# Kernel optimization log

Hardware: AMD Instinct MI355X
Metric: run time of the kernel (lower is better)

The kernel has to match this reference:

```python
import jax, jax.numpy as jnp
import numpy as np

HEADS = 16
D_MODEL = 1024
MAX_LEN = 1024
BATCH = 4
SEQ = 1024


def _skew(QEr):
    # Transformer-XL / Music-Transformer skew trick.
    # QEr: [B, H, L, L] -> pad one zero column on the left, reshape, drop first row.
    B, H, L, _ = QEr.shape
    padded = jnp.pad(QEr, ((0, 0), (0, 0), (0, 0), (1, 0)))  # [B,H,L,L+1]
    reshaped = padded.reshape(B, H, L + 1, L)
    return reshaped[:, :, 1:, :]  # [B,H,L,L]


def setup_inputs() -> dict:
    key = jax.random.key(0)
    ks = jax.random.split(key, 8)
    d = D_MODEL // HEADS
    std = 0.05  # tf.random_normal_initializer default stddev
    return {
        "query": jax.random.normal(ks[0], (BATCH, SEQ, D_MODEL), jnp.float32),
        "key": jax.random.normal(ks[1], (BATCH, SEQ, D_MODEL), jnp.float32),
        "value": jax.random.normal(ks[2], (BATCH, SEQ, D_MODEL), jnp.float32),
        "WQ": std * jax.random.normal(ks[3], (D_MODEL, D_MODEL), jnp.float32),
        "WK": std * jax.random.normal(ks[4], (D_MODEL, D_MODEL), jnp.float32),
        "WV": std * jax.random.normal(ks[5], (D_MODEL, D_MODEL), jnp.float32),
        "Er": std * jax.random.normal(ks[6], (MAX_LEN, d), jnp.float32),
        "WMerge": std * jax.random.normal(ks[7], (D_MODEL, D_MODEL), jnp.float32),
    }


def reference(query, key, value, WQ, WK, WV, Er, WMerge):
    B, L, D = query.shape
    H = HEADS
    d = D // H
    # Faithful to source: plain reshape (NOT transpose-based head split).
    q = (query @ WQ).reshape(B, H, L, d)          # [B,H,L,d]
    k_t = (key @ WK).reshape(B, H, d, L)          # [B,H,d,L]
    v = (value @ WV).reshape(B, H, L, d)          # [B,H,L,d]
    start = MAX_LEN - L
    Er_t = Er[start:, :].T                        # [d, L]
    QEr = q @ Er_t                                # [B,H,L,L]
    Srel = _skew(QEr)                             # [B,H,L,L]
    attn = (q @ k_t + Srel) / jnp.sqrt(jnp.asarray(d, q.dtype))
    attn = jax.nn.softmax(attn, axis=-1)
    out = attn @ v                                # [B,H,L,d]
    out = out.transpose(0, 2, 1, 3).reshape(B, L, D)
    return out @ WMerge
```

## Files before the change

### kernel.cpp

```cpp
#include <hip/hip_runtime.h>

#define H_  16
#define L_  1024
#define D_  1024
#define DH  64

typedef short bf16x8 __attribute__((ext_vector_type(8)));
typedef float f32x4  __attribute__((ext_vector_type(4)));

__device__ __forceinline__ ushort f2bf(float f) {
  union { float f; unsigned int u; } x; x.f = f;
  unsigned int u = x.u;
  u = (u + 0x7fffu + ((u >> 16) & 1u)) >> 16;
  return (ushort)u;
}
__device__ __forceinline__ float bf2f(ushort s) {
  union { unsigned int u; float f; } x; x.u = ((unsigned int)s) << 16;
  return x.f;
}

__global__ __launch_bounds__(256) void erF_kernel(const float* __restrict__ Er,
                                                  ushort* __restrict__ ErF) {
  int t = blockIdx.x * 256 + threadIdx.x;
  int lane = t & 63, ph = (t >> 6) & 1, jg = t >> 7;
  int m = jg * 16 + (lane & 15);
  int k = ph * 32 + (lane >> 4) * 8;
  float4 f0 = *(const float4*)(Er + m * 64 + k);
  float4 f1 = *(const float4*)(Er + m * 64 + k + 4);
  ushort4 u0, u1;
  u0.x = f2bf(f0.x); u0.y = f2bf(f0.y); u0.z = f2bf(f0.z); u0.w = f2bf(f0.w);
  u1.x = f2bf(f1.x); u1.y = f2bf(f1.y); u1.z = f2bf(f1.z); u1.w = f2bf(f1.w);
  *(ushort4*)(ErF + t * 8)     = u0;
  *(ushort4*)(ErF + t * 8 + 4) = u1;
}

__global__ __launch_bounds__(256) void wT4_kernel(
    const float* __restrict__ W0, const float* __restrict__ W1,
    const float* __restrict__ W2, const float* __restrict__ W3,
    ushort* __restrict__ T0, ushort* __restrict__ T1,
    ushort* __restrict__ T2, ushort* __restrict__ T3) {
  __shared__ ushort tt[64][72];
  const int z = blockIdx.z;
  const float* W = (z == 0) ? W0 : (z == 1) ? W1 : (z == 2) ? W2 : W3;
  ushort*     WT = (z == 0) ? T0 : (z == 1) ? T1 : (z == 2) ? T2 : T3;
  const int t = threadIdx.x;
  const int k0 = blockIdx.y * 64, n0 = blockIdx.x * 64;
#pragma unroll
  for (int c = 0; c < 4; ++c) {
    int k = c * 16 + (t >> 4);
    float4 f = *(const float4*)(W + (size_t)(k0 + k) * 1024 + n0 + (t & 15) * 4);
    tt[(t & 15) * 4 + 0][k] = f2bf(f.x);
    tt[(t & 15) * 4 + 1][k] = f2bf(f.y);
    tt[(t & 15) * 4 + 2][k] = f2bf(f.z);
    tt[(t & 15) * 4 + 3][k] = f2bf(f.w);
  }
  __syncthreads();
#pragma unroll
  for (int p = 0; p < 2; ++p) {
    int n = p * 32 + (t >> 3);
    *(uint4*)(WT + (size_t)(n0 + n) * 1024 + k0 + (t & 7) * 8) = *(const uint4*)(&tt[n][(t & 7) * 8]);
  }
}

__global__ __launch_bounds__(256) void gemm_qkv_kernel(
    const float* __restrict__ Aq, const float* __restrict__ Ak, const float* __restrict__ Av,
    const ushort* __restrict__ BTq, const ushort* __restrict__ BTk, const ushort* __restrict__ BTv,
    ushort* __restrict__ Cq, ushort* __restrict__ Ck, ushort* __restrict__ Cv) {
  __shared__ ushort lsA[128][40];
  __shared__ ushort lsB[128][40];
  const int z = blockIdx.z;
  const float*  A  = (z == 0) ? Aq  : (z == 1) ? Ak  : Av;
  const ushort* BT = (z == 0) ? BTq : (z == 1) ? BTk : BTv;
  ushort*       Cp = (z == 0) ? Cq  : (z == 1) ? Ck  : Cv;

  const int tid  = threadIdx.x;
  const int w    = tid >> 6, lane = tid & 63, qd = lane >> 4, ln = lane & 15;
  const int rw   = w >> 1, cw = w & 1;
  const int m0   = blockIdx.y * 128, n0 = blockIdx.x * 128;

  f32x4 acc[16];
#pragma unroll
  for (int i = 0; i < 16; ++i) acc[i] = (f32x4){0.f, 0.f, 0.f, 0.f};

  for (int kb = 0; kb < 32; ++kb) {
    const int k0 = kb * 32;
    {
      int row = tid >> 1, half = tid & 1;
#pragma unroll
      for (int c = 0; c < 4; ++c) {
        float4 f = *(const float4*)(A + (size_t)(m0 + row) * 1024 + k0 + half * 16 + c * 4);
        ushort4 u;
        u.x = f2bf(f.x); u.y = f2bf(f.y); u.z = f2bf(f.z); u.w = f2bf(f.w);
        *(ushort4*)(&lsA[row][half * 16 + c * 4]) = u;
      }
    }
    {
      int row = tid >> 1, half = tid & 1;
#pragma unroll
      for (int c = 0; c < 2; ++c)
        *(uint4*)(&lsB[row][half * 16 + c * 8]) =
            *(const uint4*)(BT + (size_t)(n0 + row) * 1024 + k0 + half * 16 + c * 8);
    }
    __syncthreads();
    bf16x8 afr[4], bfr[4];
#pragma unroll
    for (int am = 0; am < 4; ++am)
      afr[am] = *(const bf16x8*)(&lsA[rw * 64 + am * 16 + ln][qd * 8]);
#pragma unroll
    for (int bn = 0; bn < 4; ++bn)
      bfr[bn] = *(const bf16x8*)(&lsB[cw * 64 + bn * 16 + ln][qd * 8]);
#pragma unroll
    for (int am = 0; am < 4; ++am)
#pragma unroll
      for (int bn = 0; bn < 4; ++bn)
        acc[am * 4 + bn] = __builtin_amdgcn_mfma_f32_16x16x32_bf16(afr[am], bfr[bn], acc[am * 4 + bn], 0, 0, 0);
    __syncthreads();
  }
#pragma unroll
  for (int am = 0; am < 4; ++am)
#pragma unroll
    for (int bn = 0; bn < 4; ++bn) {
      const int rbase = m0 + rw * 64 + am * 16 + qd * 4;
      const int colg  = n0 + cw * 64 + bn * 16 + ln;
      if (z == 0) {
#pragma unroll
        for (int r = 0; r < 4; ++r)
          Cp[(size_t)(rbase + r) * 1024 + colg] = f2bf(acc[am * 4 + bn][r]);
      } else if (z == 1) {
        const int bh  = rbase >> 6;
        const int ki0 = rbase & 63;
        const int jg  = colg >> 4;
        const int ph  = ki0 >> 5;
        const int lanep = ((ki0 >> 3) & 3) * 16 + (colg & 15);
        const int jj0 = ki0 & 7;
        ushort4 u;
        u.x = f2bf(acc[am * 4 + bn][0]); u.y = f2bf(acc[am * 4 + bn][1]);
        u.z = f2bf(acc[am * 4 + bn][2]); u.w = f2bf(acc[am * 4 + bn][3]);
        *(ushort4*)(Cp + (size_t)bh * 65536 + (size_t)((jg * 2 + ph) * 64 + lanep) * 8 + jj0) = u;
      } else {
        const int bh = rbase >> 6;
        const int llow = colg >> 6, dd = colg & 63;
        const int g = dd >> 4, lnf = dd & 15;
#pragma unroll
        for (int r = 0; r < 4; ++r) {
          int l = ((rbase + r) & 63) * 16 + llow;
          int ks = l >> 5;
          int lanep = ((l >> 3) & 3) * 16 + lnf;
          int jj = l & 7;
          Cp[(size_t)bh * 65536 + (size_t)((g * 32 + ks) * 64 + lanep) * 8 + jj] = f2bf(acc[am * 4 + bn][r]);
        }
      }
    }
}

__global__ __launch_bounds__(512) void gemm_mg_kernel(const ushort* __restrict__ A,
                                                      const ushort* __restrict__ BT,
                                                      float* __restrict__ Cp) {
  __shared__ ushort ls[2][2][128][40];
  const int tid  = threadIdx.x;
  const int w    = tid >> 6, lane = tid & 63, qd = lane >> 4, ln = lane & 15;
  const int kh   = w >> 2, q = w & 3;
  const int rw   = q >> 1, cw = q & 1;
  const int m0   = blockIdx.y * 128, n0 = blockIdx.x * 128;
  const int ts   = tid >> 8, tt = tid & 255;
  const int trow = tt >> 1, thalf = tt & 1;

  f32x4 acc[16];
#pragma unroll
  for (int i = 0; i < 16; ++i) acc[i] = (f32x4){0.f, 0.f, 0.f, 0.f};

  for (int kb = 0; kb < 16; ++kb) {
    const int k0 = ts * 512 + kb * 32;
#pragma unroll
    for (int c = 0; c < 2; ++c)
      *(uint4*)(&ls[ts][0][trow][thalf * 16 + c * 8]) =
          *(const uint4*)(A + (size_t)(m0 + trow) * 1024 + k0 + thalf * 16 + c * 8);
#pragma unroll
    for (int c = 0; c < 2; ++c)
      *(uint4*)(&ls[ts][1][trow][thalf * 16 + c * 8]) =
          *(const uint4*)(BT + (size_t)(n0 + trow) * 1024 + k0 + thalf * 16 + c * 8);
    __syncthreads();
    bf16x8 afr[4], bfr[4];
#pragma unroll
    for (int am = 0; am < 4; ++am)
      afr[am] = *(const bf16x8*)(&ls[kh][0][rw * 64 + am * 16 + ln][qd * 8]);
#pragma unroll
    for (int bn = 0; bn < 4; ++bn)
      bfr[bn] = *(const bf16x8*)(&ls[kh][1][cw * 64 + bn * 16 + ln][qd * 8]);
#pragma unroll
    for (int am = 0; am < 4; ++am)
#pragma unroll
      for (int bn = 0; bn < 4; ++bn)
        acc[am * 4 + bn] = __builtin_amdgcn_mfma_f32_16x16x32_bf16(afr[am], bfr[bn], acc[am * 4 + bn], 0, 0, 0);
    __syncthreads();
  }

  float* red = (float*)&ls[0][0][0][0];
  for (int half = 0; half < 2; ++half) {
    __syncthreads();
    if (w >= 4) {
      const int base = ((w - 4) * 64 + lane) * 33;
#pragma unroll
      for (int i = 0; i < 8; ++i)
#pragma unroll
        for (int c = 0; c < 4; ++c) red[base + i * 4 + c] = acc[half * 8 + i][c];
    }
    __syncthreads();
    if (w < 4) {
      const int base = (w * 64 + lane) * 33;
#pragma unroll
      for (int i = 0; i < 8; ++i)
#pragma unroll
        for (int c = 0; c < 4; ++c) acc[half * 8 + i][c] += red[base + i * 4 + c];
    }
  }
  if (w < 4) {
#pragma unroll
    for (int am = 0; am < 4; ++am)
#pragma unroll
      for (int bn = 0; bn < 4; ++bn) {
        const int rbase = m0 + rw * 64 + am * 16 + qd * 4;
        const int colg  = n0 + cw * 64 + bn * 16 + ln;
#pragma unroll
        for (int r = 0; r < 4; ++r)
          Cp[(size_t)(rbase + r) * 1024 + colg] = acc[am * 4 + bn][r];
      }
  }
}

__global__ __launch_bounds__(512, 4) void attn_kernel(
    const ushort* __restrict__ QW, const ushort* __restrict__ KF,
    const ushort* __restrict__ VF, const ushort* __restrict__ ErF,
    ushort* __restrict__ Om) {
  __shared__ ushort qp[17][1032];
  __shared__ float  red[4][64][4];
  __shared__ float  stats[2][8][16];

  const int tid  = threadIdx.x;
  const int w    = tid >> 6;
  const int lane = tid & 63;
  const int qd   = lane >> 4;
  const int ln   = lane & 15;
  const int bh   = blockIdx.y;
  const int i0   = blockIdx.x << 4;
  const ushort* q  = QW + ((size_t)bh << 16);
  const ushort* kf = KF + ((size_t)bh << 16);
  const ushort* vf = VF + ((size_t)bh << 16);

  bf16x8 a00 = *(const bf16x8*)(q + (size_t)(i0 + ln) * 64 + qd * 8);
  bf16x8 a01 = *(const bf16x8*)(q + (size_t)(i0 + ln) * 64 + 32 + qd * 8);
  const int row16 = (i0 + 16 > 1023) ? 1023 : i0 + 16;
  bf16x8 a10 = *(const bf16x8*)(q + (size_t)row16 * 64 + qd * 8);
  bf16x8 a11 = *(const bf16x8*)(q + (size_t)row16 * 64 + 32 + qd * 8);

  const int jg0 = w * 8;

#pragma unroll
  for (int f = 0; f < 8; ++f) {
    const int jg = jg0 + f;
    bf16x8 b0 = *(const bf16x8*)(ErF + (size_t)((jg * 2 + 0) * 64 + lane) * 8);
    bf16x8 b1 = *(const bf16x8*)(ErF + (size_t)((jg * 2 + 1) * 64 + lane) * 8);
    f32x4 acc = {0.f, 0.f, 0.f, 0.f};
    acc = __builtin_amdgcn_mfma_f32_16x16x32_bf16(a00, b0, acc, 0, 0, 0);
    acc = __builtin_amdgcn_mfma_f32_16x16x32_bf16(a01, b1, acc, 0, 0, 0);
    const int m = jg * 16 + ln;
#pragma unroll
    for (int r = 0; r < 4; ++r) qp[qd * 4 + r][m] = f2bf(acc[r]);
    if (jg * 16 <= 1006 - i0) {
      f32x4 ac2 = {0.f, 0.f, 0.f, 0.f};
      ac2 = __builtin_amdgcn_mfma_f32_16x16x32_bf16(a10, b0, ac2, 0, 0, 0);
      ac2 = __builtin_amdgcn_mfma_f32_16x16x32_bf16(a11, b1, ac2, 0, 0, 0);
      if (qd == 0) qp[16][m] = f2bf(ac2[0]);
    }
  }

  f32x4 sfr[8];
#pragma unroll
  for (int f = 0; f < 8; ++f) {
    const int jg = jg0 + f;
    bf16x8 b0 = *(const bf16x8*)(kf + (size_t)((jg * 2 + 0) * 64 + lane) * 8);
    bf16x8 b1 = *(const bf16x8*)(kf + (size_t)((jg * 2 + 1) * 64 + lane) * 8);
    f32x4 acc = {0.f, 0.f, 0.f, 0.f};
    acc = __builtin_amdgcn_mfma_f32_16x16x32_bf16(a00, b0, acc, 0, 0, 0);
    acc = __builtin_amdgcn_mfma_f32_16x16x32_bf16(a01, b1, acc, 0, 0, 0);
    sfr[f] = acc;
  }
  __syncthreads();

#pragma unroll
  for (int f = 0; f < 8; ++f) {
    const int j = w * 128 + f * 16 + ln;
#pragma unroll
    for (int r = 0; r < 4; ++r) {
      int rloc = qd * 4 + r;
      int i = i0 + rloc;
      float srel;
      if (j <= i)          srel = bf2f(qp[rloc][1023 - i + j]);
      else if (j == i + 1) srel = 0.f;
      else                 srel = bf2f(qp[rloc + 1][j - i - 2]);
      sfr[f][r] = (sfr[f][r] + srel) * 0.125f;
    }
  }

  {
    float vm[4];
#pragma unroll
    for (int r = 0; r < 4; ++r) {
      float m = sfr[0][r];
#pragma unroll
      for (int f = 1; f < 8; ++f) m = fmaxf(m, sfr[f][r]);
#pragma unroll
      for (int off = 1; off < 16; off <<= 1) m = fmaxf(m, __shfl_xor(m, off, 64));
      vm[r] = m;
    }
    if (ln == 0) {
#pragma unroll
      for (int r = 0; r < 4; ++r) stats[0][w][qd * 4 + r] = vm[r];
    }
  }
  __syncthreads();
  float gm[4];
#pragma unroll
  for (int r = 0; r < 4; ++r) {
    float m = stats[0][0][qd * 4 + r];
#pragma unroll
    for (int ww = 1; ww < 8; ++ww) m = fmaxf(m, stats[0][ww][qd * 4 + r]);
    gm[r] = m;
  }

  float vs[4] = {0.f, 0.f, 0.f, 0.f};
#pragma unroll
  for (int f = 0; f < 8; ++f) {
    const int j = w * 128 + f * 16 + ln;
#pragma unroll
    for (int r = 0; r < 4; ++r) {
      float e = __expf(sfr[f][r] - gm[r]);
      vs[r] += e;
      qp[qd * 4 + r][j] = f2bf(e);
    }
  }
#pragma unroll
  for (int r = 0; r < 4; ++r) {
    float s = vs[r];
#pragma unroll
    for (int off = 1; off < 16; off <<= 1) s += __shfl_xor(s, off, 64);
    if (ln == 0) stats[1][w][qd * 4 + r] = s;
  }
  __syncthreads();
  float rrl[4];
#pragma unroll
  for (int r = 0; r < 4; ++r) {
    float s = 0.f;
#pragma unroll
    for (int ww = 0; ww < 8; ++ww) s += stats[1][ww][qd * 4 + r];
    rrl[r] = 1.0f / s;
  }

  const int g = w & 3, kh = w >> 2;
  f32x4 oacc = {0.f, 0.f, 0.f, 0.f};
#pragma unroll
  for (int kc = 0; kc < 16; ++kc) {
    const int ks = kh * 16 + kc;
    bf16x8 ap = *(const bf16x8*)(&qp[ln][ks * 32 + qd * 8]);
    bf16x8 bv = *(const bf16x8*)(vf + (size_t)((g * 32 + ks) * 64 + lane) * 8);
    oacc = __builtin_amdgcn_mfma_f32_16x16x32_bf16(ap, bv, oacc, 0, 0, 0);
  }

  if (w >= 4) {
#pragma unroll
    for (int cc = 0; cc < 4; ++cc) red[w - 4][lane][cc] = oacc[cc];
  }
  __syncthreads();
  if (w < 4) {
    const int b = bh >> 4, h = bh & 15;
    ushort* ob = Om + ((size_t)b * L_ * D_) + (size_t)h * DH + (size_t)(g * 16 + ln);
#pragma unroll
    for (int r = 0; r < 4; ++r) {
      float o = oacc[r] + red[w][lane][r];
      int row = i0 + qd * 4 + r;
      ob[(size_t)row * D_] = f2bf(o * rrl[r]);
    }
  }
}

extern "C" void kernel_launch(void* const* d_in, const int* in_sizes, int n_in,
                              void* d_out, int out_size, void* d_ws, size_t ws_size,
                              hipStream_t stream) {
  const float* query = (const float*)d_in[0];
  const float* key   = (const float*)d_in[1];
  const float* value = (const float*)d_in[2];
  const float* WQ    = (const float*)d_in[3];
  const float* WK    = (const float*)d_in[4];
  const float* WV    = (const float*)d_in[5];
  const float* Er    = (const float*)d_in[6];
  const float* WM    = (const float*)d_in[7];
  float* out = (float*)d_out;

  ushort* QW  = (ushort*)d_ws;
  ushort* KF  = QW  + (size_t)4096 * 1024;
  ushort* VF  = KF  + (size_t)4096 * 1024;
  ushort* O   = VF  + (size_t)4096 * 1024;
  ushort* ErF = O   + (size_t)4096 * 1024;
  ushort* WTQ = ErF + (size_t)65536;
  ushort* WTK = WTQ + (size_t)1024 * 1024;
  ushort* WTV = WTK + (size_t)1024 * 1024;
  ushort* WTM = WTV + (size_t)1024 * 1024;

  wT4_kernel<<<dim3(16, 16, 4), 256, 0, stream>>>(WQ, WK, WV, WM, WTQ, WTK, WTV, WTM);
  erF_kernel<<<32, 256, 0, stream>>>(Er, ErF);

  gemm_qkv_kernel<<<dim3(8, 32, 3), 256, 0, stream>>>(query, key, value,
                                                      WTQ, WTK, WTV,
                                                      QW, KF, VF);

  attn_kernel<<<dim3(64, 64), 512, 0, stream>>>(QW, KF, VF, ErF, O);

  gemm_mg_kernel<<<dim3(8, 32), 512, 0, stream>>>(O, WTM, out);
}
```

Baseline: 308.9 us.

## Pre-convert QKV inputs to bf16 and simplify skewed relative-score indexing

Adds a separate kernel that converts query/key/value to bf16 once, so the QKV GEMM loads bf16 A tiles directly instead of reading fp32 and converting inside the k-loop. In the attention kernel, the relative-position buffer is stored with a row stride of 1025 plus a zero pad, so the skew becomes a single flat-index load without branches. The softmax uses exp2 with the 1/sqrt(d) scale folded into one fma. The cost is an extra kernel launch and an extra bf16 round trip through global memory for the inputs.

```diff
diff --git a/kernel.cpp b/kernel.cpp
--- a/kernel.cpp
+++ b/kernel.cpp
@@ -17,6 +17,20 @@
 __device__ __forceinline__ float bf2f(ushort s) {
   union { unsigned int u; float f; } x; x.u = ((unsigned int)s) << 16;
   return x.f;
+}
+
+__global__ __launch_bounds__(256) void cvt3_kernel(
+    const float* __restrict__ q, const float* __restrict__ k, const float* __restrict__ v,
+    ushort* __restrict__ qb, ushort* __restrict__ kb, ushort* __restrict__ vb) {
+  const int z = blockIdx.y;
+  const float* in = (z == 0) ? q : (z == 1) ? k : v;
+  ushort* out = (z == 0) ? qb : (z == 1) ? kb : vb;
+  int i = (blockIdx.x * 256 + threadIdx.x) * 8;
+  float4 f0 = *(const float4*)(in + i);
+  float4 f1 = *(const float4*)(in + i + 4);
+  ushort u[8] = {f2bf(f0.x), f2bf(f0.y), f2bf(f0.z), f2bf(f0.w),
+                 f2bf(f1.x), f2bf(f1.y), f2bf(f1.z), f2bf(f1.w)};
+  *(uint4*)(out + i) = *(uint4*)u;
 }
 
 __global__ __launch_bounds__(256) void erF_kernel(const float* __restrict__ Er,
@@ -63,13 +77,13 @@
 }
 
 __global__ __launch_bounds__(256) void gemm_qkv_kernel(
-    const float* __restrict__ Aq, const float* __restrict__ Ak, const float* __restrict__ Av,
+    const ushort* __restrict__ Aq, const ushort* __restrict__ Ak, const ushort* __restrict__ Av,
     const ushort* __restrict__ BTq, const ushort* __restrict__ BTk, const ushort* __restrict__ BTv,
     ushort* __restrict__ Cq, ushort* __restrict__ Ck, ushort* __restrict__ Cv) {
   __shared__ ushort lsA[128][40];
   __shared__ ushort lsB[128][40];
   const int z = blockIdx.z;
-  const float*  A  = (z == 0) ? Aq  : (z == 1) ? Ak  : Av;
+  const ushort* A  = (z == 0) ? Aq  : (z == 1) ? Ak  : Av;
   const ushort* BT = (z == 0) ? BTq : (z == 1) ? BTk : BTv;
   ushort*       Cp = (z == 0) ? Cq  : (z == 1) ? Ck  : Cv;
 
@@ -84,23 +98,15 @@
 
   for (int kb = 0; kb < 32; ++kb) {
     const int k0 = kb * 32;
-    {
-      int row = tid >> 1, half = tid & 1;
-#pragma unroll
-      for (int c = 0; c < 4; ++c) {
-        float4 f = *(const float4*)(A + (size_t)(m0 + row) * 1024 + k0 + half * 16 + c * 4);
-        ushort4 u;
-        u.x = f2bf(f.x); u.y = f2bf(f.y); u.z = f2bf(f.z); u.w = f2bf(f.w);
-        *(ushort4*)(&lsA[row][half * 16 + c * 4]) = u;
-      }
-    }
-    {
-      int row = tid >> 1, half = tid & 1;
-#pragma unroll
-      for (int c = 0; c < 2; ++c)
-        *(uint4*)(&lsB[row][half * 16 + c * 8]) =
-            *(const uint4*)(BT + (size_t)(n0 + row) * 1024 + k0 + half * 16 + c * 8);
-    }
+    const int row = tid >> 1, half = tid & 1;
+#pragma unroll
+    for (int c = 0; c < 2; ++c)
+      *(uint4*)(&lsA[row][half * 16 + c * 8]) =
+          *(const uint4*)(A + (size_t)(m0 + row) * 1024 + k0 + half * 16 + c * 8);
+#pragma unroll
+    for (int c = 0; c < 2; ++c)
+      *(uint4*)(&lsB[row][half * 16 + c * 8]) =
+          *(const uint4*)(BT + (size_t)(n0 + row) * 1024 + k0 + half * 16 + c * 8);
     __syncthreads();
     bf16x8 afr[4], bfr[4];
 #pragma unroll
@@ -232,7 +238,7 @@
     const ushort* __restrict__ QW, const ushort* __restrict__ KF,
     const ushort* __restrict__ VF, const ushort* __restrict__ ErF,
     ushort* __restrict__ Om) {
-  __shared__ ushort qp[17][1032];
+  __shared__ ushort qflat[17440];
   __shared__ float  red[4][64][4];
   __shared__ float  stats[2][8][16];
 
@@ -247,6 +253,8 @@
   const ushort* kf = KF + ((size_t)bh << 16);
   const ushort* vf = VF + ((size_t)bh << 16);
 
+  if (tid < 16) qflat[tid * 1025 + 1024] = 0;
+
   bf16x8 a00 = *(const bf16x8*)(q + (size_t)(i0 + ln) * 64 + qd * 8);
   bf16x8 a01 = *(const bf16x8*)(q + (size_t)(i0 + ln) * 64 + 32 + qd * 8);
   const int row16 = (i0 + 16 > 1023) ? 1023 : i0 + 16;
@@ -265,12 +273,12 @@
     acc = __builtin_amdgcn_mfma_f32_16x16x32_bf16(a01, b1, acc, 0, 0, 0);
     const int m = jg * 16 + ln;
 #pragma unroll
-    for (int r = 0; r < 4; ++r) qp[qd * 4 + r][m] = f2bf(acc[r]);
+    for (int r = 0; r < 4; ++r) qflat[(qd * 4 + r) * 1025 + m] = f2bf(acc[r]);
     if (jg * 16 <= 1006 - i0) {
       f32x4 ac2 = {0.f, 0.f, 0.f, 0.f};
       ac2 = __builtin_amdgcn_mfma_f32_16x16x32_bf16(a10, b0, ac2, 0, 0, 0);
       ac2 = __builtin_amdgcn_mfma_f32_16x16x32_bf16(a11, b1, ac2, 0, 0, 0);
-      if (qd == 0) qp[16][m] = f2bf(ac2[0]);
+      if (qd == 0) qflat[16 * 1025 + m] = f2bf(ac2[0]);
     }
   }
 
@@ -289,17 +297,10 @@
 
 #pragma unroll
   for (int f = 0; f < 8; ++f) {
-    const int j = w * 128 + f * 16 + ln;
-#pragma unroll
-    for (int r = 0; r < 4; ++r) {
-      int rloc = qd * 4 + r;
-      int i = i0 + rloc;
-      float srel;
-      if (j <= i)          srel = bf2f(qp[rloc][1023 - i + j]);
-      else if (j == i + 1) srel = 0.f;
-      else                 srel = bf2f(qp[rloc + 1][j - i - 2]);
-      sfr[f][r] = (sfr[f][r] + srel) * 0.125f;
-    }
+    const int cj = 1023 - i0 + w * 128 + f * 16 + ln;
+#pragma unroll
+    for (int r = 0; r < 4; ++r)
+      sfr[f][r] += bf2f(qflat[(qd * 4 + r) * 1024 + cj]);
   }
 
   {
@@ -319,13 +320,14 @@
     }
   }
   __syncthreads();
-  float gm[4];
+  const float cexp = 0.18033688011112042f;
+  float gm2[4];
 #pragma unroll
   for (int r = 0; r < 4; ++r) {
     float m = stats[0][0][qd * 4 + r];
 #pragma unroll
     for (int ww = 1; ww < 8; ++ww) m = fmaxf(m, stats[0][ww][qd * 4 + r]);
-    gm[r] = m;
+    gm2[r] = -m * cexp;
   }
 
   float vs[4] = {0.f, 0.f, 0.f, 0.f};
@@ -334,9 +336,9 @@
     const int j = w * 128 + f * 16 + ln;
 #pragma unroll
     for (int r = 0; r < 4; ++r) {
-      float e = __expf(sfr[f][r] - gm[r]);
+      float e = exp2f(fmaf(sfr[f][r], cexp, gm2[r]));
       vs[r] += e;
-      qp[qd * 4 + r][j] = f2bf(e);
+      qflat[(qd * 4 + r) * 1048 + j] = f2bf(e);
     }
   }
 #pragma unroll
@@ -361,7 +363,7 @@
 #pragma unroll
   for (int kc = 0; kc < 16; ++kc) {
     const int ks = kh * 16 + kc;
-    bf16x8 ap = *(const bf16x8*)(&qp[ln][ks * 32 + qd * 8]);
+    bf16x8 ap = *(const bf16x8*)(qflat + ln * 1048 + ks * 32 + qd * 8);
     bf16x8 bv = *(const bf16x8*)(vf + (size_t)((g * 32 + ks) * 64 + lane) * 8);
     oacc = __builtin_amdgcn_mfma_f32_16x16x32_bf16(ap, bv, oacc, 0, 0, 0);
   }
@@ -405,11 +407,15 @@
   ushort* WTK = WTQ + (size_t)1024 * 1024;
   ushort* WTV = WTK + (size_t)1024 * 1024;
   ushort* WTM = WTV + (size_t)1024 * 1024;
-
+  ushort* KB  = WTM + (size_t)1024 * 1024;
+  ushort* VB  = KB  + (size_t)4096 * 1024;
+  ushort* QB  = O;
+
+  cvt3_kernel<<<dim3(2048, 3), 256, 0, stream>>>(query, key, value, QB, KB, VB);
   wT4_kernel<<<dim3(16, 16, 4), 256, 0, stream>>>(WQ, WK, WV, WM, WTQ, WTK, WTV, WTM);
   erF_kernel<<<32, 256, 0, stream>>>(Er, ErF);
 
-  gemm_qkv_kernel<<<dim3(8, 32, 3), 256, 0, stream>>>(query, key, value,
+  gemm_qkv_kernel<<<dim3(8, 32, 3), 256, 0, stream>>>(QB, KB, VB,
                                                       WTQ, WTK, WTV,
                                                       QW, KF, VF);
 
```

New measurement: 298.0 us. 1.04x faster.
